# Performance work log

Measured on AMD Instinct MI355X. Metric: run time of the kernel, lower is better.

The kernel has to match this reference:

```python
import jax, jax.numpy as jnp
import numpy as np

B, S, ENC, DEC = 64, 4096, 512, 512


def setup_inputs() -> dict:
    key = jax.random.key(0)
    k1, k2, k3 = jax.random.split(key, 3)
    decoderFeature = jax.random.normal(k1, (B, 1, DEC), dtype=jnp.float32)
    encoderFeature = jax.random.normal(k2, (B, S, ENC), dtype=jnp.float32)
    # xavier_uniform for W: [enc, dec]
    limit = float(np.sqrt(6.0 / (ENC + DEC)))
    W = jax.random.uniform(k3, (ENC, DEC), dtype=jnp.float32, minval=-limit, maxval=limit)
    return {"decoderFeature": decoderFeature, "encoderFeature": encoderFeature, "W": W}


def reference(decoderFeature, encoderFeature, W):
    # F.linear(x, W) = x @ W.T : [B,1,dec] -> [B,1,enc]
    sub = jnp.einsum('bqd,ed->bqe', decoderFeature, W)
    # scores: [B,1,S]
    attn = jnp.einsum('bqe,bse->bqs', sub, encoderFeature)
    attn = jax.nn.softmax(attn, axis=2)
    # weighted sum: [B, enc]
    sumResult = jnp.einsum('bqs,bse->bqe', attn, encoderFeature).reshape(attn.shape[0], -1)
    return attn, sumResult
```

## Files before the change

### kernel.cpp

```cpp
#include <hip/hip_runtime.h>
#include <math.h>

#define BB   64
#define SS   4096
#define ENC  512
#define DEC  512
#define NSPLIT 32
#define CHUNK (SS / NSPLIT)

__global__ __launch_bounds__(256) void k_sub(const float* __restrict__ dec,
                                             const float* __restrict__ W,
                                             float* __restrict__ sub) {
    const int b    = blockIdx.y;
    const int lane = threadIdx.x & 63;
    const int wave = threadIdx.x >> 6;

    const float4* dv = (const float4*)(dec + (size_t)b * DEC);
    float4 q0 = dv[lane];
    float4 q1 = dv[lane + 64];

    const int e0 = blockIdx.x * 128 + wave * 32;
    for (int i = 0; i < 32; ++i) {
        const int e = e0 + i;
        const float4* wv = (const float4*)(W + (size_t)e * DEC);
        float4 w0 = wv[lane];
        float4 w1 = wv[lane + 64];
        float p = q0.x * w0.x + q0.y * w0.y + q0.z * w0.z + q0.w * w0.w
                + q1.x * w1.x + q1.y * w1.y + q1.z * w1.z + q1.w * w1.w;
        #pragma unroll
        for (int off = 32; off >= 1; off >>= 1) p += __shfl_xor(p, off, 64);
        if (lane == 0) sub[(size_t)b * ENC + e] = p;
    }
}

__global__ __launch_bounds__(256) void k_attn(const float* __restrict__ enc,
                                              const float* __restrict__ sub,
                                              float* __restrict__ attn_raw,
                                              float* __restrict__ chunk_m,
                                              float* __restrict__ chunk_l,
                                              float* __restrict__ chunk_acc) {
    const int b    = blockIdx.y;
    const int c    = blockIdx.x;
    const int lane = threadIdx.x & 63;
    const int wave = threadIdx.x >> 6;

    const float4* qv = (const float4*)(sub + (size_t)b * ENC);
    float4 q0 = qv[lane];
    float4 q1 = qv[lane + 64];

    const int rowBase = c * CHUNK + wave * 32;
    const float4* base = (const float4*)(enc + ((size_t)b * SS + rowBase) * ENC);

    float m = -INFINITY, l = 0.f;
    float4 a0 = {0, 0, 0, 0}, a1 = {0, 0, 0, 0};

    float4 buf[2][4][2];
    #pragma unroll
    for (int r = 0; r < 4; ++r) {
        const float4* ev = base + (size_t)r * (ENC / 4);
        buf[0][r][0] = ev[lane];
        buf[0][r][1] = ev[lane + 64];
    }

    #pragma unroll
    for (int j = 0; j < 8; ++j) {
        const int cb = j & 1;
        const int nb = cb ^ 1;
        if (j < 7) {
            #pragma unroll
            for (int r = 0; r < 4; ++r) {
                const float4* ev = base + (size_t)(4 * (j + 1) + r) * (ENC / 4);
                buf[nb][r][0] = ev[lane];
                buf[nb][r][1] = ev[lane + 64];
            }
        }

        float p0, p1, p2, p3;
        {
            const float4 e0 = buf[cb][0][0], e1 = buf[cb][0][1];
            p0 = q0.x * e0.x + q0.y * e0.y + q0.z * e0.z + q0.w * e0.w
               + q1.x * e1.x + q1.y * e1.y + q1.z * e1.z + q1.w * e1.w;
        }
        {
            const float4 e0 = buf[cb][1][0], e1 = buf[cb][1][1];
            p1 = q0.x * e0.x + q0.y * e0.y + q0.z * e0.z + q0.w * e0.w
               + q1.x * e1.x + q1.y * e1.y + q1.z * e1.z + q1.w * e1.w;
        }
        {
            const float4 e0 = buf[cb][2][0], e1 = buf[cb][2][1];
            p2 = q0.x * e0.x + q0.y * e0.y + q0.z * e0.z + q0.w * e0.w
               + q1.x * e1.x + q1.y * e1.y + q1.z * e1.z + q1.w * e1.w;
        }
        {
            const float4 e0 = buf[cb][3][0], e1 = buf[cb][3][1];
            p3 = q0.x * e0.x + q0.y * e0.y + q0.z * e0.z + q0.w * e0.w
               + q1.x * e1.x + q1.y * e1.y + q1.z * e1.z + q1.w * e1.w;
        }

        float s0, s1, s2, s3;
        {
            const float tA = __shfl_xor(p0, 32, 64);
            const float tB = __shfl_xor(p1, 32, 64);
            float u = (lane < 32) ? (p0 + tA) : (p1 + tB);
            #pragma unroll
            for (int off = 16; off >= 1; off >>= 1) u += __shfl_xor(u, off, 64);
            const float v = __shfl_xor(u, 32, 64);
            s0 = (lane < 32) ? u : v;
            s1 = (lane < 32) ? v : u;
        }
        {
            const float tA = __shfl_xor(p2, 32, 64);
            const float tB = __shfl_xor(p3, 32, 64);
            float u = (lane < 32) ? (p2 + tA) : (p3 + tB);
            #pragma unroll
            for (int off = 16; off >= 1; off >>= 1) u += __shfl_xor(u, off, 64);
            const float v = __shfl_xor(u, 32, 64);
            s2 = (lane < 32) ? u : v;
            s3 = (lane < 32) ? v : u;
        }

        if (lane == 0) {
            *(float4*)&attn_raw[(size_t)b * SS + rowBase + 4 * j] =
                make_float4(s0, s1, s2, s3);
        }

        const float mt = fmaxf(fmaxf(s0, s1), fmaxf(s2, s3));
        const float mn = fmaxf(m, mt);
        const float sc = __expf(m - mn);
        const float w0 = __expf(s0 - mn);
        const float w1 = __expf(s1 - mn);
        const float w2 = __expf(s2 - mn);
        const float w3 = __expf(s3 - mn);
        l = l * sc + ((w0 + w1) + (w2 + w3));

        const float4 e00 = buf[cb][0][0], e01 = buf[cb][0][1];
        const float4 e10 = buf[cb][1][0], e11 = buf[cb][1][1];
        const float4 e20 = buf[cb][2][0], e21 = buf[cb][2][1];
        const float4 e30 = buf[cb][3][0], e31 = buf[cb][3][1];

        a0.x = a0.x * sc + w0 * e00.x + w1 * e10.x + w2 * e20.x + w3 * e30.x;
        a0.y = a0.y * sc + w0 * e00.y + w1 * e10.y + w2 * e20.y + w3 * e30.y;
        a0.z = a0.z * sc + w0 * e00.z + w1 * e10.z + w2 * e20.z + w3 * e30.z;
        a0.w = a0.w * sc + w0 * e00.w + w1 * e10.w + w2 * e20.w + w3 * e30.w;
        a1.x = a1.x * sc + w0 * e01.x + w1 * e11.x + w2 * e21.x + w3 * e31.x;
        a1.y = a1.y * sc + w0 * e01.y + w1 * e11.y + w2 * e21.y + w3 * e31.y;
        a1.z = a1.z * sc + w0 * e01.z + w1 * e11.z + w2 * e21.z + w3 * e31.z;
        a1.w = a1.w * sc + w0 * e01.w + w1 * e11.w + w2 * e21.w + w3 * e31.w;

        m = mn;
    }

    __shared__ float sm[4];
    __shared__ float sl[4];
    __shared__ float sacc[4][ENC];

    if (lane == 0) sm[wave] = m;
    __syncthreads();
    const float M = fmaxf(fmaxf(sm[0], sm[1]), fmaxf(sm[2], sm[3]));
    const float f = __expf(m - M);
    if (lane == 0) sl[wave] = l * f;
    float* sa = &sacc[wave][0];
    sa[4 * lane + 0]       = a0.x * f;  sa[4 * lane + 1]       = a0.y * f;
    sa[4 * lane + 2]       = a0.z * f;  sa[4 * lane + 3]       = a0.w * f;
    sa[256 + 4 * lane + 0] = a1.x * f;  sa[256 + 4 * lane + 1] = a1.y * f;
    sa[256 + 4 * lane + 2] = a1.z * f;  sa[256 + 4 * lane + 3] = a1.w * f;
    __syncthreads();

    const size_t idx = (size_t)b * NSPLIT + c;
    if (threadIdx.x == 0) {
        chunk_m[idx] = M;
        chunk_l[idx] = sl[0] + sl[1] + sl[2] + sl[3];
    }
    for (int e = threadIdx.x; e < ENC; e += 256) {
        chunk_acc[idx * ENC + e] = sacc[0][e] + sacc[1][e] + sacc[2][e] + sacc[3][e];
    }
}

__global__ __launch_bounds__(256) void k_final(const float* __restrict__ chunk_m,
                                               const float* __restrict__ chunk_l,
                                               const float* __restrict__ chunk_acc,
                                               float* __restrict__ attn,
                                               float* __restrict__ sumResult) {
    const int b = blockIdx.x;
    const int y = blockIdx.y;

    float M = -INFINITY;
    #pragma unroll
    for (int c = 0; c < NSPLIT; ++c) M = fmaxf(M, chunk_m[(size_t)b * NSPLIT + c]);
    float L = 0.f;
    #pragma unroll
    for (int c = 0; c < NSPLIT; ++c)
        L += chunk_l[(size_t)b * NSPLIT + c] * __expf(chunk_m[(size_t)b * NSPLIT + c] - M);
    const float invL = 1.f / L;

    if (y == 0) {
        float f[NSPLIT];
        #pragma unroll
        for (int c = 0; c < NSPLIT; ++c)
            f[c] = __expf(chunk_m[(size_t)b * NSPLIT + c] - M);
        for (int e = threadIdx.x; e < ENC; e += 256) {
            float s = 0.f;
            #pragma unroll
            for (int c = 0; c < NSPLIT; ++c)
                s += chunk_acc[((size_t)b * NSPLIT + c) * ENC + e] * f[c];
            sumResult[(size_t)b * ENC + e] = s * invL;
        }
    }

    const int s0 = y * (SS / NSPLIT);
    for (int s = s0 + threadIdx.x; s < s0 + SS / NSPLIT; s += 256) {
        const size_t i = (size_t)b * SS + s;
        attn[i] = __expf(attn[i] - M) * invL;
    }
}

extern "C" void kernel_launch(void* const* d_in, const int* in_sizes, int n_in,
                              void* d_out, int out_size, void* d_ws, size_t ws_size,
                              hipStream_t stream) {
    const float* dec = (const float*)d_in[0];
    const float* enc = (const float*)d_in[1];
    const float* W   = (const float*)d_in[2];

    float* out       = (float*)d_out;
    float* attn      = out;
    float* sumResult = out + (size_t)BB * SS;

    float* ws        = (float*)d_ws;
    float* sub       = ws;
    float* chunk_m   = sub + (size_t)BB * ENC;
    float* chunk_l   = chunk_m + (size_t)BB * NSPLIT;
    float* chunk_acc = chunk_l + (size_t)BB * NSPLIT;

    k_sub  <<<dim3(4, BB),       256, 0, stream>>>(dec, W, sub);
    k_attn <<<dim3(NSPLIT, BB),  256, 0, stream>>>(enc, sub, attn, chunk_m, chunk_l, chunk_acc);
    k_final<<<dim3(BB, NSPLIT),  256, 0, stream>>>(chunk_m, chunk_l, chunk_acc, attn, sumResult);
}
```

Measured before the change: 703.4 us.

## Drop intra-block LDS merge; write per-wave softmax partials and merge in final kernel

Each wave in the attention kernel now writes its own running max, sum and accumulator vector straight to global memory. This removes the shared-memory reduction and both __syncthreads. The final kernel merges 128 partials per batch instead of 32, uses shared exp factors, and runs with 8 blocks per batch instead of 32. k_sub is split into more, smaller blocks for more parallelism. The cost is four times more partial-accumulator traffic, about 16 MB written and read back, plus longer per-thread loops in the final kernel.

Result: slower. 721.6 us (+2.6%).

```diff
diff --git a/kernel.cpp b/kernel.cpp
--- a/kernel.cpp
+++ b/kernel.cpp
@@ -7,6 +7,8 @@
 #define DEC  512
 #define NSPLIT 32
 #define CHUNK (SS / NSPLIT)
+#define NP   (NSPLIT * 4)
+#define NFIN 8
 
 __global__ __launch_bounds__(256) void k_sub(const float* __restrict__ dec,
                                              const float* __restrict__ W,
@@ -19,8 +21,8 @@
     float4 q0 = dv[lane];
     float4 q1 = dv[lane + 64];
 
-    const int e0 = blockIdx.x * 128 + wave * 32;
-    for (int i = 0; i < 32; ++i) {
+    const int e0 = blockIdx.x * 32 + wave * 8;
+    for (int i = 0; i < 8; ++i) {
         const int e = e0 + i;
         const float4* wv = (const float4*)(W + (size_t)e * DEC);
         float4 w0 = wv[lane];
@@ -36,19 +38,20 @@
 __global__ __launch_bounds__(256) void k_attn(const float* __restrict__ enc,
                                               const float* __restrict__ sub,
                                               float* __restrict__ attn_raw,
-                                              float* __restrict__ chunk_m,
-                                              float* __restrict__ chunk_l,
-                                              float* __restrict__ chunk_acc) {
+                                              float* __restrict__ part_m,
+                                              float* __restrict__ part_l,
+                                              float* __restrict__ part_acc) {
     const int b    = blockIdx.y;
     const int c    = blockIdx.x;
     const int lane = threadIdx.x & 63;
     const int wave = threadIdx.x >> 6;
+    const int part = c * 4 + wave;
 
     const float4* qv = (const float4*)(sub + (size_t)b * ENC);
     float4 q0 = qv[lane];
     float4 q1 = qv[lane + 64];
 
-    const int rowBase = c * CHUNK + wave * 32;
+    const int rowBase = part * 32;
     const float4* base = (const float4*)(enc + ((size_t)b * SS + rowBase) * ENC);
 
     float m = -INFINITY, l = 0.f;
@@ -150,65 +153,49 @@
         m = mn;
     }
 
-    __shared__ float sm[4];
-    __shared__ float sl[4];
-    __shared__ float sacc[4][ENC];
-
-    if (lane == 0) sm[wave] = m;
-    __syncthreads();
-    const float M = fmaxf(fmaxf(sm[0], sm[1]), fmaxf(sm[2], sm[3]));
-    const float f = __expf(m - M);
-    if (lane == 0) sl[wave] = l * f;
-    float* sa = &sacc[wave][0];
-    sa[4 * lane + 0]       = a0.x * f;  sa[4 * lane + 1]       = a0.y * f;
-    sa[4 * lane + 2]       = a0.z * f;  sa[4 * lane + 3]       = a0.w * f;
-    sa[256 + 4 * lane + 0] = a1.x * f;  sa[256 + 4 * lane + 1] = a1.y * f;
-    sa[256 + 4 * lane + 2] = a1.z * f;  sa[256 + 4 * lane + 3] = a1.w * f;
-    __syncthreads();
-
-    const size_t idx = (size_t)b * NSPLIT + c;
-    if (threadIdx.x == 0) {
-        chunk_m[idx] = M;
-        chunk_l[idx] = sl[0] + sl[1] + sl[2] + sl[3];
-    }
-    for (int e = threadIdx.x; e < ENC; e += 256) {
-        chunk_acc[idx * ENC + e] = sacc[0][e] + sacc[1][e] + sacc[2][e] + sacc[3][e];
-    }
-}
-
-__global__ __launch_bounds__(256) void k_final(const float* __restrict__ chunk_m,
-                                               const float* __restrict__ chunk_l,
-                                               const float* __restrict__ chunk_acc,
+    const size_t idx = (size_t)b * NP + part;
+    if (lane == 0) {
+        part_m[idx] = m;
+        part_l[idx] = l;
+    }
+    float* pa = part_acc + idx * ENC;
+    *(float4*)(pa + 4 * lane)       = a0;
+    *(float4*)(pa + 256 + 4 * lane) = a1;
+}
+
+__global__ __launch_bounds__(256) void k_final(const float* __restrict__ part_m,
+                                               const float* __restrict__ part_l,
+                                               const float* __restrict__ part_acc,
                                                float* __restrict__ attn,
                                                float* __restrict__ sumResult) {
     const int b = blockIdx.x;
     const int y = blockIdx.y;
 
+    __shared__ float fs[NP];
+
     float M = -INFINITY;
-    #pragma unroll
-    for (int c = 0; c < NSPLIT; ++c) M = fmaxf(M, chunk_m[(size_t)b * NSPLIT + c]);
+    for (int c = 0; c < NP; ++c) M = fmaxf(M, part_m[(size_t)b * NP + c]);
     float L = 0.f;
-    #pragma unroll
-    for (int c = 0; c < NSPLIT; ++c)
-        L += chunk_l[(size_t)b * NSPLIT + c] * __expf(chunk_m[(size_t)b * NSPLIT + c] - M);
+    for (int c = 0; c < NP; ++c)
+        L += part_l[(size_t)b * NP + c] * __expf(part_m[(size_t)b * NP + c] - M);
     const float invL = 1.f / L;
 
+    if (threadIdx.x < NP)
+        fs[threadIdx.x] = __expf(part_m[(size_t)b * NP + threadIdx.x] - M);
+    __syncthreads();
+
     if (y == 0) {
-        float f[NSPLIT];
-        #pragma unroll
-        for (int c = 0; c < NSPLIT; ++c)
-            f[c] = __expf(chunk_m[(size_t)b * NSPLIT + c] - M);
         for (int e = threadIdx.x; e < ENC; e += 256) {
             float s = 0.f;
-            #pragma unroll
-            for (int c = 0; c < NSPLIT; ++c)
-                s += chunk_acc[((size_t)b * NSPLIT + c) * ENC + e] * f[c];
+            #pragma unroll 8
+            for (int c = 0; c < NP; ++c)
+                s = fmaf(part_acc[((size_t)b * NP + c) * ENC + e], fs[c], s);
             sumResult[(size_t)b * ENC + e] = s * invL;
         }
     }
 
-    const int s0 = y * (SS / NSPLIT);
-    for (int s = s0 + threadIdx.x; s < s0 + SS / NSPLIT; s += 256) {
+    const int s0 = y * (SS / NFIN);
+    for (int s = s0 + threadIdx.x; s < s0 + SS / NFIN; s += 256) {
         const size_t i = (size_t)b * SS + s;
         attn[i] = __expf(attn[i] - M) * invL;
     }
@@ -227,11 +214,11 @@
 
     float* ws        = (float*)d_ws;
     float* sub       = ws;
-    float* chunk_m   = sub + (size_t)BB * ENC;
-    float* chunk_l   = chunk_m + (size_t)BB * NSPLIT;
-    float* chunk_acc = chunk_l + (size_t)BB * NSPLIT;
-
-    k_sub  <<<dim3(4, BB),       256, 0, stream>>>(dec, W, sub);
-    k_attn <<<dim3(NSPLIT, BB),  256, 0, stream>>>(enc, sub, attn, chunk_m, chunk_l, chunk_acc);
-    k_final<<<dim3(BB, NSPLIT),  256, 0, stream>>>(chunk_m, chunk_l, chunk_acc, attn, sumResult);
-}
+    float* part_m    = sub + (size_t)BB * ENC;
+    float* part_l    = part_m + (size_t)BB * NP;
+    float* part_acc  = part_l + (size_t)BB * NP;
+
+    k_sub  <<<dim3(16, BB),      256, 0, stream>>>(dec, W, sub);
+    k_attn <<<dim3(NSPLIT, BB),  256, 0, stream>>>(enc, sub, attn, part_m, part_l, part_acc);
+    k_final<<<dim3(BB, NFIN),    256, 0, stream>>>(part_m, part_l, part_acc, attn, sumResult);
+}
```
